# Kernel optimization log

Hardware: AMD Instinct MI355X
Metric: run time of the kernel (lower is better)

The kernel has to match this reference:

```python
import jax, jax.numpy as jnp
import numpy as np

EMBED_DIM = 1024
NUM_HEADS = 16
HEAD_DIM = EMBED_DIM // NUM_HEADS
SCALE = HEAD_DIM ** -0.5


def setup_inputs() -> dict:
    key = jax.random.key(0)
    ks = jax.random.split(key, 5)
    B, N, D = 8, 1024, EMBED_DIM
    std = D ** -0.5
    x = jax.random.normal(ks[0], (B, N, D), dtype=jnp.float32)
    W_qkv = jax.random.normal(ks[1], (D, 3 * D), dtype=jnp.float32) * std
    b_qkv = jnp.zeros((3 * D,), dtype=jnp.float32)
    W_proj = jax.random.normal(ks[2], (D, D), dtype=jnp.float32) * std
    b_proj = jnp.zeros((D,), dtype=jnp.float32)
    return {"x": x, "W_qkv": W_qkv, "b_qkv": b_qkv, "W_proj": W_proj, "b_proj": b_proj}


def reference(x, W_qkv, b_qkv, W_proj, b_proj):
    B, N, D = x.shape
    H, hd = NUM_HEADS, HEAD_DIM
    # QKV projection: (B,N,3D) -> (3,B,H,N,hd)
    qkv = (x @ W_qkv + b_qkv).reshape(B, N, 3, H, hd).transpose(2, 0, 3, 1, 4)
    q, k, v = qkv[0], qkv[1], qkv[2]
    # scaled dot-product attention, full (B,H,N,N) scores as in original
    attn = jnp.einsum('bhqd,bhkd->bhqk', q, k) * SCALE
    attn = jax.nn.softmax(attn, axis=-1)
    out = jnp.einsum('bhqk,bhkd->bhqd', attn, v)  # (B,H,N,hd)
    out = out.transpose(0, 2, 1, 3).reshape(B, N, D)
    return out @ W_proj + b_proj
```

## Files before the change

kernel.cpp:

```cpp
#include <hip/hip_runtime.h>

#define AS1(p) ((const __attribute__((address_space(1))) void*)(p))
#define AS3(p) ((__attribute__((address_space(3))) void*)(p))

typedef __attribute__((ext_vector_type(8))) short bf16x8;
typedef __attribute__((ext_vector_type(4))) float f32x4;
typedef __attribute__((ext_vector_type(16))) float f32x16;

static constexpr int kBatch = 8;
static constexpr int kSeq = 1024;
static constexpr int kD = 1024;
static constexpr int kH = 16;
static constexpr int kHD = 64;
static constexpr int kRows = kBatch * kSeq;
static constexpr int kQKVCols = 3 * kD;

__device__ __forceinline__ unsigned short f2bf(float f) {
  union { float f; unsigned int u; } a; a.f = f;
  unsigned int r = a.u + 0x7fffu + ((a.u >> 16) & 1u);
  return (unsigned short)(r >> 16);
}

__device__ __forceinline__ unsigned pkbf(float a, float b) {
  unsigned r;
  asm("v_cvt_pk_bf16_f32 %0, %1, %2" : "=v"(r) : "v"(a), "v"(b));
  return r;
}

__device__ __forceinline__ int swap23(int x) {
  return (x & ~12) | ((x & 4) << 1) | ((x & 8) >> 1);
}

__global__ __launch_bounds__(256) void prep_kernel(
    const float* __restrict__ x, unsigned short* __restrict__ Xbf,
    const float* __restrict__ Wqkv, unsigned short* __restrict__ WqkvT,
    const float* __restrict__ Wproj, unsigned short* __restrict__ WpT) {
  const int bid = blockIdx.x, t = threadIdx.x;
  if (bid < 1024) {
    const int n4 = kRows * kD / 4;
    int i = bid * 256 + t;
    const int stride = 1024 * 256;
    for (; i < n4; i += stride) {
      float4 v = reinterpret_cast<const float4*>(x)[i];
      ushort4 o;
      o.x = f2bf(v.x); o.y = f2bf(v.y); o.z = f2bf(v.z); o.w = f2bf(v.w);
      reinterpret_cast<ushort4*>(Xbf)[i] = o;
    }
    return;
  }
  __shared__ float tile[32][33];
  const float* W; unsigned short* Wt; int cols, c0, r0;
  if (bid < 4096) {
    const int idx = bid - 1024;
    W = Wqkv; Wt = WqkvT; cols = kQKVCols;
    c0 = (idx % 96) * 32; r0 = (idx / 96) * 32;
  } else {
    const int idx = bid - 4096;
    W = Wproj; Wt = WpT; cols = kD;
    c0 = (idx % 32) * 32; r0 = (idx / 32) * 32;
  }
  const int tx = t & 31, ty = t >> 5;
#pragma unroll
  for (int i = 0; i < 32; i += 8)
    tile[ty + i][tx] = W[(size_t)(r0 + ty + i) * cols + (c0 + tx)];
  __syncthreads();
#pragma unroll
  for (int i = 0; i < 32; i += 8)
    Wt[(size_t)(c0 + ty + i) * 1024 + (r0 + tx)] = f2bf(tile[tx][ty + i]);
}

__global__ __launch_bounds__(256) void vtrans_kernel(
    const unsigned short* __restrict__ qkv, unsigned short* __restrict__ Vt) {
  __shared__ alignas(16) unsigned short tile[64][72];
  const int nt = blockIdx.x, bh = blockIdx.y;
  const int b = bh >> 4, h = bh & 15;
  const unsigned short* Vb = qkv + (size_t)b * kSeq * kQKVCols + 2 * kD + h * kHD;
  const int t = threadIdx.x;
#pragma unroll
  for (int r = 0; r < 2; ++r) {
    const int c = r * 256 + t;
    const int n = c >> 3, d8 = c & 7;
    uint4 v = *reinterpret_cast<const uint4*>(Vb + (size_t)(nt * 64 + n) * kQKVCols + d8 * 8);
    *reinterpret_cast<uint4*>(&tile[n][d8 * 8]) = v;
  }
  __syncthreads();
#pragma unroll
  for (int r = 0; r < 2; ++r) {
    const int c = r * 256 + t;
    const int d = c >> 3, n8 = c & 7;
    unsigned short w8[8];
#pragma unroll
    for (int j = 0; j < 8; ++j) w8[j] = tile[swap23(n8 * 8 + j)][d];
    *reinterpret_cast<uint4*>(Vt + (size_t)bh * kHD * kSeq + (size_t)d * kSeq + nt * 64 + n8 * 8) =
        *reinterpret_cast<uint4*>(w8);
  }
}

template <int MODE>
__global__ __launch_bounds__(256) void gemm_bt_kernel(
    const unsigned short* __restrict__ A,
    const unsigned short* __restrict__ Bt,
    const float* __restrict__ bias,
    void* __restrict__ Cout, unsigned short* __restrict__ Vt,
    int M, int Nn, int K) {
  constexpr int BK = 64;
  __shared__ alignas(16) unsigned short As[128 * BK];
  __shared__ alignas(16) unsigned short Bs[128 * BK];
  const int t = threadIdx.x;
  const int lane = t & 63;
  const int w = t >> 6;
  const int wr = w >> 1, wc = w & 1;
  const int l15 = lane & 15, lhi = lane >> 4;
  const int nwg = gridDim.x * gridDim.y;
  const int lin = blockIdx.y * gridDim.x + blockIdx.x;
  const int swz = (lin & 7) * (nwg >> 3) + (lin >> 3);
  const int row0 = (swz / gridDim.x) * 128;
  const int col0 = (swz % gridDim.x) * 128;

  f32x4 acc[4][4] = {};
  const int ldsb = (t & ~63) * 16;

  for (int k0 = 0; k0 < K; k0 += BK) {
    __syncthreads();
#pragma unroll
    for (int r = 0; r < 4; ++r) {
      int c = r * 256 + t;
      int arow = c >> 3;
      int ccol = ((c & 7) ^ (arow & 7)) * 8;
      const unsigned short* ga = A + (size_t)(row0 + arow) * K + (k0 + ccol);
      const unsigned short* gb = Bt + (size_t)(col0 + arow) * K + (k0 + ccol);
      char* la = (char*)As + r * 4096 + ldsb;
      char* lb = (char*)Bs + r * 4096 + ldsb;
      __builtin_amdgcn_global_load_lds(AS1(ga), AS3(la), 16, 0, 0);
      __builtin_amdgcn_global_load_lds(AS1(gb), AS3(lb), 16, 0, 0);
    }
    __syncthreads();
#pragma unroll
    for (int kk = 0; kk < 2; ++kk) {
      bf16x8 af[4], bfr[4];
#pragma unroll
      for (int mi = 0; mi < 4; ++mi) {
        int rowa = wr * 64 + mi * 16 + l15;
        int chunk = (kk * 4 + lhi) ^ (rowa & 7);
        af[mi] = *reinterpret_cast<const bf16x8*>((const char*)As + rowa * 128 + chunk * 16);
      }
#pragma unroll
      for (int ni = 0; ni < 4; ++ni) {
        int rowb = wc * 64 + ni * 16 + l15;
        int chunk = (kk * 4 + lhi) ^ (rowb & 7);
        bfr[ni] = *reinterpret_cast<const bf16x8*>((const char*)Bs + rowb * 128 + chunk * 16);
      }
#pragma unroll
      for (int mi = 0; mi < 4; ++mi)
#pragma unroll
        for (int ni = 0; ni < 4; ++ni)
          acc[mi][ni] = __builtin_amdgcn_mfma_f32_16x16x32_bf16(af[mi], bfr[ni], acc[mi][ni], 0, 0, 0);
    }
  }

  if (MODE == 3) {
#pragma unroll
    for (int mi = 0; mi < 4; ++mi) {
      const int rbase = row0 + wr * 64 + mi * 16 + lhi * 4;
      const int b = rbase >> 10, n = rbase & 1023;
      const int nbase = (n & ~63) | swap23(n & 63);
#pragma unroll
      for (int ni = 0; ni < 4; ++ni) {
        const int col = col0 + wc * 64 + ni * 16 + l15;
        const int hv = col >> 6;
        const int d = col & 63;
        const float bv = bias[col];
        uint2 uu;
        uu.x = pkbf(acc[mi][ni][0] + bv, acc[mi][ni][1] + bv);
        uu.y = pkbf(acc[mi][ni][2] + bv, acc[mi][ni][3] + bv);
        *reinterpret_cast<uint2*>(Vt + ((size_t)((b << 4) + hv) << 16) + d * 1024 + nbase) = uu;
      }
    }
    return;
  }

#pragma unroll
  for (int mi = 0; mi < 4; ++mi) {
    int rbase = row0 + wr * 64 + mi * 16 + lhi * 4;
#pragma unroll
    for (int ni = 0; ni < 4; ++ni) {
      int col = col0 + wc * 64 + ni * 16 + l15;
      float bv = bias[col];
#pragma unroll
      for (int j = 0; j < 4; ++j) {
        float v = acc[mi][ni][j] + bv;
        if (MODE != 0)
          ((unsigned short*)Cout)[(size_t)(rbase + j) * Nn + col] = f2bf(v);
        else
          ((float*)Cout)[(size_t)(rbase + j) * Nn + col] = v;
      }
    }
  }
}

#define G256_STAGE_A(BUF, HALF, KT)                                           \
  do {                                                                        \
    char* _d = smem + (BUF) * 65536 + (HALF) * 16384 + ldst;                  \
    const unsigned short* _s0 = Ap + aoff0 + (size_t)(HALF) * halfstep + (KT) * 64; \
    const unsigned short* _s1 = Ap + aoff1 + (size_t)(HALF) * halfstep + (KT) * 64; \
    __builtin_amdgcn_global_load_lds(AS1(_s0), AS3(_d), 16, 0, 0);            \
    __builtin_amdgcn_global_load_lds(AS1(_s1), AS3(_d + 8192), 16, 0, 0);     \
  } while (0)
#define G256_STAGE_B(BUF, HALF, KT)                                           \
  do {                                                                        \
    char* _d = smem + (BUF) * 65536 + 32768 + (HALF) * 16384 + ldst;          \
    const unsigned short* _s0 = Bp + boff0 + (size_t)(HALF) * halfstep + (KT) * 64; \
    const unsigned short* _s1 = Bp + boff1 + (size_t)(HALF) * halfstep + (KT) * 64; \
    __builtin_amdgcn_global_load_lds(AS1(_s0), AS3(_d), 16, 0, 0);            \
    __builtin_amdgcn_global_load_lds(AS1(_s1), AS3(_d + 8192), 16, 0, 0);     \
  } while (0)
#define G256_PHASE(RBUF, QM, QN, STAGE_STMT, DO_VM)                           \
  do {                                                                        \
    const char* _Ab = smem + (RBUF) * 65536 + (QM) * 16384;                   \
    const char* _Bb = smem + (RBUF) * 65536 + 32768 + (QN) * 16384;           \
    bf16x8 _af[2][4], _bf[2][2];                                              \
    _Pragma("unroll") for (int kk = 0; kk < 2; ++kk) {                        \
      _Pragma("unroll") for (int mi = 0; mi < 4; ++mi) {                      \
        const int rr = wm * 64 + mi * 16 + l15;                               \
        const int ch = (kk * 4 + lhi) ^ (rr & 7);                             \
        _af[kk][mi] = *reinterpret_cast<const bf16x8*>(_Ab + rr * 128 + ch * 16); \
      }                                                                       \
      _Pragma("unroll") for (int ni = 0; ni < 2; ++ni) {                      \
        const int rr = wn * 32 + ni * 16 + l15;                               \
        const int ch = (kk * 4 + lhi) ^ (rr & 7);                             \
        _bf[kk][ni] = *reinterpret_cast<const bf16x8*>(_Bb + rr * 128 + ch * 16); \
      }                                                                       \
    }                                                                         \
    STAGE_STMT;                                                               \
    if (DO_VM) asm volatile("s_waitcnt vmcnt(4)" ::: "memory");               \
    asm volatile("" ::: "memory");                                            \
    __builtin_amdgcn_s_barrier();                                             \
    asm volatile("s_waitcnt lgkmcnt(0)" ::: "memory");                        \
    __builtin_amdgcn_sched_barrier(0);                                        \
    __builtin_amdgcn_s_setprio(1);                                            \
    _Pragma("unroll") for (int kk = 0; kk < 2; ++kk)                          \
      _Pragma("unroll") for (int mi = 0; mi < 4; ++mi)                        \
        _Pragma("unroll") for (int ni = 0; ni < 2; ++ni)                      \
          acc[QM][QN][mi][ni] = __builtin_amdgcn_mfma_f32_16x16x32_bf16(      \
              _af[kk][mi], _bf[kk][ni], acc[QM][QN][mi][ni], 0, 0, 0);        \
    __builtin_amdgcn_s_setprio(0);                                            \
    asm volatile("" ::: "memory");                                            \
    __builtin_amdgcn_s_barrier();                                             \
    asm volatile("" ::: "memory");                                            \
  } while (0)

__global__ __launch_bounds__(512, 2) void gemm256_kernel(
    const unsigned short* __restrict__ Ap,
    const unsigned short* __restrict__ Bp,
    const float* __restrict__ bias,
    unsigned short* __restrict__ Cout, int M, int Nn, int K) {
  __shared__ alignas(16) char smem[131072];
  const int t = threadIdx.x;
  const int lane = t & 63;
  const int wid = t >> 6;
  const int wm = wid >> 2, wn = wid & 3;
  const int l15 = lane & 15, lhi = lane >> 4;

  const int nwg = gridDim.x * gridDim.y;
  const int lin = blockIdx.y * gridDim.x + blockIdx.x;
  const int swz = (lin & 7) * (nwg >> 3) + (lin >> 3);
  const int row0 = (swz / gridDim.x) * 256;
  const int col0 = (swz % gridDim.x) * 256;

  const int r0i = t >> 3, r1i = (512 + t) >> 3;
  const int sc0 = ((t & 7) ^ (r0i & 7)) * 8;
  const int sc1 = (((512 + t) & 7) ^ (r1i & 7)) * 8;
  const size_t aoff0 = (size_t)(row0 + r0i) * K + sc0;
  const size_t aoff1 = (size_t)(row0 + r1i) * K + sc1;
  const size_t boff0 = (size_t)(col0 + r0i) * K + sc0;
  const size_t boff1 = (size_t)(col0 + r1i) * K + sc1;
  const size_t halfstep = (size_t)128 * K;
  const int ldst = (t & ~63) * 16;

  f32x4 acc[2][2][4][2] = {};

  G256_STAGE_A(0, 0, 0);
  G256_STAGE_B(0, 1, 0);
  G256_STAGE_A(0, 1, 0);
  G256_STAGE_B(0, 0, 0);
  G256_STAGE_A(1, 0, 1);
  G256_STAGE_B(1, 1, 1);
  asm volatile("s_waitcnt vmcnt(4)" ::: "memory");
  __builtin_amdgcn_s_barrier();
  asm volatile("" ::: "memory");

  const int nkt = K >> 6;
  const int niter = nkt >> 1;
  for (int i = 0; i < niter; ++i) {
    const int tc1 = 2 * i + 1;
    const int tn0 = (2 * i + 2) & (nkt - 1);
    const int tn1 = (2 * i + 3) & (nkt - 1);
    G256_PHASE(0, 0, 0, G256_STAGE_A(1, 1, tc1), 0);
    G256_PHASE(0, 0, 1, G256_STAGE_B(1, 0, tc1), 0);
    G256_PHASE(0, 1, 1, G256_STAGE_A(0, 0, tn0), 0);
    G256_PHASE(0, 1, 0, G256_STAGE_B(0, 1, tn0), 1);
    G256_PHASE(1, 0, 0, G256_STAGE_A(0, 1, tn0), 0);
    G256_PHASE(1, 0, 1, G256_STAGE_B(0, 0, tn0), 0);
    G256_PHASE(1, 1, 1, G256_STAGE_A(1, 0, tn1), 0);
    G256_PHASE(1, 1, 0, G256_STAGE_B(1, 1, tn1), 1);
  }

#pragma unroll
  for (int qm = 0; qm < 2; ++qm)
#pragma unroll
    for (int mi = 0; mi < 4; ++mi) {
      const int rbase = row0 + qm * 128 + wm * 64 + mi * 16 + lhi * 4;
#pragma unroll
      for (int qn = 0; qn < 2; ++qn)
#pragma unroll
        for (int ni = 0; ni < 2; ++ni) {
          const int col = col0 + qn * 128 + wn * 32 + ni * 16 + l15;
          const float bv = bias[col];
#pragma unroll
          for (int j = 0; j < 4; ++j) {
            const float v = acc[qm][qn][mi][ni][j] + bv;
            Cout[(size_t)(rbase + j) * Nn + col] = f2bf(v);
          }
        }
    }
}

__global__ __launch_bounds__(512, 4) void attn_kernel(
    const unsigned short* __restrict__ qkv,
    const unsigned short* __restrict__ Vt,
    unsigned short* __restrict__ ctx) {
  __shared__ alignas(16) char smem[32768];
  const int lin = blockIdx.x;
  const int swz = (lin & 7) * 64 + (lin >> 3);
  const int bh = swz >> 2, qt = swz & 3;
  const int b = bh >> 4, h = bh & 15;
  const int t = threadIdx.x, lane = t & 63, w = t >> 6;
  const int l31 = lane & 31, hi = lane >> 5;

  const unsigned short* Qb = qkv + (size_t)b * kSeq * kQKVCols + h * kHD;
  const unsigned short* Kb = Qb + kD;
  const unsigned short* Vtb = Vt + (size_t)bh * kHD * kSeq;

  bf16x8 qf[4];
  const int qrow = qt * 256 + w * 32 + l31;
#pragma unroll
  for (int s = 0; s < 4; ++s)
    qf[s] = *reinterpret_cast<const bf16x8*>(Qb + (size_t)qrow * kQKVCols + s * 16 + hi * 8);

  const int srow = t >> 3;
  const int sc = ((t & 7) ^ (srow & 7)) * 8;
  const unsigned short* gk = Kb + (size_t)srow * kQKVCols + sc;
  const unsigned short* gv = Vtb + (size_t)srow * kSeq + sc;
  const int ldst = w * 1024;

  auto stage = [&](int bufb) {
    __builtin_amdgcn_global_load_lds(AS1(gk), AS3(smem + bufb + ldst), 16, 0, 0);
    __builtin_amdgcn_global_load_lds(AS1(gv), AS3(smem + bufb + 8192 + ldst), 16, 0, 0);
    gk += 64 * kQKVCols;
    gv += 64;
  };

  f32x16 oacc[2] = {};
  float lrun = 0.f;
  constexpr float kSc = 0.125f * 1.44269504f;

  stage(0);
  __syncthreads();
  int cur = 0;
  for (int kt = 0; kt < 16; ++kt) {
    if (kt < 15) stage((cur ^ 1) * 16384);
    const char* Kp = smem + cur * 16384;
    const char* Vp = Kp + 8192;

    f32x16 sacc[2] = {};
    __builtin_amdgcn_s_setprio(1);
#pragma unroll
    for (int nb = 0; nb < 2; ++nb) {
      const int n = nb * 32 + l31;
#pragma unroll
      for (int s = 0; s < 4; ++s) {
        const int ch = (s * 2 + hi) ^ (n & 7);
        bf16x8 kf = *reinterpret_cast<const bf16x8*>(Kp + n * 128 + ch * 16);
        sacc[nb] = __builtin_amdgcn_mfma_f32_32x32x16_bf16(kf, qf[s], sacc[nb], 0, 0, 0);
      }
    }
    __builtin_amdgcn_s_setprio(0);

    float ps0 = 0.f, ps1 = 0.f, ps2 = 0.f, ps3 = 0.f;
#pragma unroll
    for (int nb = 0; nb < 2; ++nb)
#pragma unroll
      for (int r = 0; r < 16; ++r) {
        const float e = __builtin_amdgcn_exp2f(sacc[nb][r] * kSc);
        sacc[nb][r] = e;
        if ((r & 3) == 0) ps0 += e;
        else if ((r & 3) == 1) ps1 += e;
        else if ((r & 3) == 2) ps2 += e;
        else ps3 += e;
      }
    float ps = (ps0 + ps1) + (ps2 + ps3);
    lrun += ps + __shfl_xor(ps, 32, 64);

    bf16x8 pf[4];
#pragma unroll
    for (int s = 0; s < 4; ++s) {
      const int nb = s >> 1, h2 = (s & 1) * 8;
      union { unsigned u[4]; bf16x8 v; } pk4;
#pragma unroll
      for (int i = 0; i < 4; ++i)
        pk4.u[i] = pkbf(sacc[nb][h2 + 2 * i], sacc[nb][h2 + 2 * i + 1]);
      pf[s] = pk4.v;
    }

    __builtin_amdgcn_s_setprio(1);
#pragma unroll
    for (int db = 0; db < 2; ++db) {
      const int dr = db * 32 + l31;
#pragma unroll
      for (int s = 0; s < 4; ++s) {
        const int ch = (s * 2 + hi) ^ (dr & 7);
        bf16x8 vf = *reinterpret_cast<const bf16x8*>(Vp + dr * 128 + ch * 16);
        oacc[db] = __builtin_amdgcn_mfma_f32_32x32x16_bf16(vf, pf[s], oacc[db], 0, 0, 0);
      }
    }
    __builtin_amdgcn_s_setprio(0);
    __syncthreads();
    cur ^= 1;
  }

  const float rl = 1.0f / lrun;
  const int qlocal = w * 32 + l31;
#pragma unroll
  for (int db = 0; db < 2; ++db)
#pragma unroll
    for (int g = 0; g < 4; ++g) {
      const unsigned u0 = pkbf(oacc[db][g * 4 + 0] * rl, oacc[db][g * 4 + 1] * rl);
      const unsigned u1 = pkbf(oacc[db][g * 4 + 2] * rl, oacc[db][g * 4 + 3] * rl);
      const int ch = db * 4 + g;
      uint2 uu; uu.x = u0; uu.y = u1;
      *reinterpret_cast<uint2*>(smem + qlocal * 128 + ((ch ^ (qlocal & 7)) * 16) + hi * 8) = uu;
    }
  __syncthreads();
#pragma unroll
  for (int it = 0; it < 4; ++it) {
    const int idx = it * 512 + t;
    const int row = idx >> 3, ch = idx & 7;
    const uint4 vv = *reinterpret_cast<const uint4*>(smem + row * 128 + ((ch ^ (row & 7)) * 16));
    *reinterpret_cast<uint4*>(ctx + (size_t)(b * kSeq + qt * 256 + row) * kD + h * kHD + ch * 8) = vv;
  }
}

extern "C" void kernel_launch(void* const* d_in, const int* in_sizes, int n_in,
                              void* d_out, int out_size, void* d_ws, size_t ws_size,
                              hipStream_t stream) {
  const float* x     = (const float*)d_in[0];
  const float* Wqkv  = (const float*)d_in[1];
  const float* bqkv  = (const float*)d_in[2];
  const float* Wproj = (const float*)d_in[3];
  const float* bproj = (const float*)d_in[4];
  float* out = (float*)d_out;

  char* ws = (char*)d_ws;
  size_t oXbf   = 0;
  size_t oWqkvT = oXbf   + (size_t)kRows * kD * 2;
  size_t oWpT   = oWqkvT + (size_t)kQKVCols * kD * 2;
  size_t oQKV   = oWpT   + (size_t)kD * kD * 2;
  size_t oCTX   = oQKV   + (size_t)kRows * kQKVCols * 2;
  size_t oVt    = oCTX   + (size_t)kRows * kD * 2;
  size_t total_base  = oVt;
  size_t total_fused = oVt + (size_t)kRows * kD * 2;
  if (ws_size < total_base) return;
  const bool fused_vt = ws_size >= total_fused;

  unsigned short* Xbf   = (unsigned short*)(ws + oXbf);
  unsigned short* WqkvT = (unsigned short*)(ws + oWqkvT);
  unsigned short* WpT   = (unsigned short*)(ws + oWpT);
  unsigned short* QKV   = (unsigned short*)(ws + oQKV);
  unsigned short* CTX   = (unsigned short*)(ws + oCTX);
  unsigned short* VtF   = (unsigned short*)(ws + oVt);
  unsigned short* VtA   = (unsigned short*)(ws + oXbf);

  prep_kernel<<<5120, 256, 0, stream>>>(x, Xbf, Wqkv, WqkvT, Wproj, WpT);
  if (fused_vt) {
    gemm256_kernel<<<dim3(2048 / 256, kRows / 256), 512, 0, stream>>>(
        Xbf, WqkvT, bqkv, QKV, kRows, kQKVCols, kD);
    gemm_bt_kernel<3><<<dim3(1024 / 128, kRows / 128), 256, 0, stream>>>(
        Xbf, WqkvT + (size_t)2048 * kD, bqkv + 2048, nullptr, VtF,
        kRows, 1024, kD);
    attn_kernel<<<512, 512, 0, stream>>>(QKV, VtF, CTX);
  } else {
    gemm_bt_kernel<1><<<dim3(kQKVCols / 128, kRows / 128), 256, 0, stream>>>(
        Xbf, WqkvT, bqkv, QKV, nullptr, kRows, kQKVCols, kD);
    vtrans_kernel<<<dim3(16, 128), 256, 0, stream>>>(QKV, VtA);
    attn_kernel<<<512, 512, 0, stream>>>(QKV, VtA, CTX);
  }
  gemm_bt_kernel<0><<<dim3(kD / 128, kRows / 128), 256, 0, stream>>>(
      CTX, WpT, bproj, out, nullptr, kRows, kD, kD);
}
```

Before: 145.3 us.

## Fold softmax scale into Q projection and compute row sums via MFMA

Pre-multiplies the Q columns of the QKV projection output by scale*log2(e) in the GEMM epilogue, so the attention kernel drops the per-element multiply before exp2. The per-row softmax denominator is now accumulated by an extra MFMA of a ones vector against the bf16 probability tiles, replacing the scalar adds and cross-lane shuffle. This moves VALU work onto the matrix cores, but costs four extra MFMAs per tile, extra accumulator registers, and sums the bf16-rounded probabilities rather than the fp32 ones.

```diff
diff --git a/kernel.cpp b/kernel.cpp
--- a/kernel.cpp
+++ b/kernel.cpp
@@ -14,6 +14,7 @@
 static constexpr int kHD = 64;
 static constexpr int kRows = kBatch * kSeq;
 static constexpr int kQKVCols = 3 * kD;
+#define KSC_ATTN 0.1803368801111204f
 
 __device__ __forceinline__ unsigned short f2bf(float f) {
   union { float f; unsigned int u; } a; a.f = f;
@@ -186,9 +187,10 @@
     for (int ni = 0; ni < 4; ++ni) {
       int col = col0 + wc * 64 + ni * 16 + l15;
       float bv = bias[col];
+      const float qs = (MODE == 1 && col < 1024) ? KSC_ATTN : 1.0f;
 #pragma unroll
       for (int j = 0; j < 4; ++j) {
-        float v = acc[mi][ni][j] + bv;
+        float v = (acc[mi][ni][j] + bv) * qs;
         if (MODE != 0)
           ((unsigned short*)Cout)[(size_t)(rbase + j) * Nn + col] = f2bf(v);
         else
@@ -316,9 +318,10 @@
         for (int ni = 0; ni < 2; ++ni) {
           const int col = col0 + qn * 128 + wn * 32 + ni * 16 + l15;
           const float bv = bias[col];
+          const float qs = (col < 1024) ? KSC_ATTN : 1.0f;
 #pragma unroll
           for (int j = 0; j < 4; ++j) {
-            const float v = acc[qm][qn][mi][ni][j] + bv;
+            const float v = (acc[qm][qn][mi][ni][j] + bv) * qs;
             Cout[(size_t)(rbase + j) * Nn + col] = f2bf(v);
           }
         }
@@ -347,6 +350,10 @@
   for (int s = 0; s < 4; ++s)
     qf[s] = *reinterpret_cast<const bf16x8*>(Qb + (size_t)qrow * kQKVCols + s * 16 + hi * 8);
 
+  bf16x8 ones;
+#pragma unroll
+  for (int i = 0; i < 8; ++i) ones[i] = (short)0x3F80;
+
   const int srow = t >> 3;
   const int sc = ((t & 7) ^ (srow & 7)) * 8;
   const unsigned short* gk = Kb + (size_t)srow * kQKVCols + sc;
@@ -361,9 +368,7 @@
   };
 
   f32x16 oacc[2] = {};
-  float lrun = 0.f;
-  constexpr float kSc = 0.125f * 1.44269504f;
-
+  f32x16 lacc = {};
   stage(0);
   __syncthreads();
   int cur = 0;
@@ -386,20 +391,11 @@
     }
     __builtin_amdgcn_s_setprio(0);
 
-    float ps0 = 0.f, ps1 = 0.f, ps2 = 0.f, ps3 = 0.f;
 #pragma unroll
     for (int nb = 0; nb < 2; ++nb)
 #pragma unroll
-      for (int r = 0; r < 16; ++r) {
-        const float e = __builtin_amdgcn_exp2f(sacc[nb][r] * kSc);
-        sacc[nb][r] = e;
-        if ((r & 3) == 0) ps0 += e;
-        else if ((r & 3) == 1) ps1 += e;
-        else if ((r & 3) == 2) ps2 += e;
-        else ps3 += e;
-      }
-    float ps = (ps0 + ps1) + (ps2 + ps3);
-    lrun += ps + __shfl_xor(ps, 32, 64);
+      for (int r = 0; r < 16; ++r)
+        sacc[nb][r] = __builtin_amdgcn_exp2f(sacc[nb][r]);
 
     bf16x8 pf[4];
 #pragma unroll
@@ -423,12 +419,15 @@
         oacc[db] = __builtin_amdgcn_mfma_f32_32x32x16_bf16(vf, pf[s], oacc[db], 0, 0, 0);
       }
     }
+#pragma unroll
+    for (int s = 0; s < 4; ++s)
+      lacc = __builtin_amdgcn_mfma_f32_32x32x16_bf16(ones, pf[s], lacc, 0, 0, 0);
     __builtin_amdgcn_s_setprio(0);
     __syncthreads();
     cur ^= 1;
   }
 
-  const float rl = 1.0f / lrun;
+  const float rl = 1.0f / lacc[0];
   const int qlocal = w * 32 + l31;
 #pragma unroll
   for (int db = 0; db < 2; ++db)
```

Measured after the change: 146.5 us (median of 2 runs). Within noise of the previous version (+0.9%).
